# Kernel tuning notes

Measured on AMD Instinct MI355X. Metric: run time of the kernel, lower is better.

## Reference

```python
import jax, jax.numpy as jnp
import numpy as np

V = 4          # view_num
B = 2048       # batch_size
D = 512        # feature dim
N = V * B
TEMP = 0.5     # temperature
EPS = 1e-8     # torch CosineSimilarity eps


def _neg_idx():
    # Row with residue p (position within its view block) masks out columns c
    # with c % B == p (the positive/self positions), exactly matching
    # mask_positive_samples: fill_diagonal_(0) on every BxB block.
    cols = np.arange(N)
    return np.stack([cols[cols % B != p] for p in range(B)])  # [B, N-V]

_NEG_IDX = jnp.asarray(_neg_idx())


def setup_inputs() -> dict:
    key = jax.random.key(0)
    x = jax.random.normal(key, (V, B, D), dtype=jnp.float32)
    return {"x": x}


def reference(x):
    # torch.cat(input, dim=0) -> [N, D]
    xf = x.reshape(N, D)
    # Cosine similarity via normalize + matmul (same math as broadcasted
    # CosineSimilarity(dim=2), expressed efficiently).
    norm = jnp.maximum(jnp.linalg.norm(xf, axis=1, keepdims=True), EPS)
    xn = xf / norm
    sim = (xn @ xn.T) / TEMP                                  # [N, N]

    # Negatives per anchor row: gather masked columns (same column order as
    # torch boolean-mask indexing, which is row-major ascending).
    sim_v = sim.reshape(V, B, N)
    negs = jnp.take_along_axis(sim_v, _NEG_IDX[None], axis=2)  # [V, B, N-V]
    lse_neg = jax.nn.logsumexp(negs, axis=2)                   # [V, B]

    # pos[i, j, b] = sim block-diagonal between views i and j
    pos = jnp.diagonal(sim.reshape(V, B, V, B), axis1=1, axis2=3)  # [V, V, B]

    # CrossEntropy with label 0 on logits = [pos_ij, negatives_i]:
    #   loss_b = logsumexp([pos, negs]) - pos = logaddexp(pos, lse_neg) - pos
    lse = jnp.logaddexp(pos, lse_neg[:, None, :])              # [V, V, B]
    per_pair = (lse - pos).sum(axis=2) / B                     # [V, V]

    off_diag = 1.0 - jnp.eye(V, dtype=per_pair.dtype)          # skip j == i
    return jnp.sum(per_pair * off_diag)
```

## Files before the change

kernel.cpp:

```cpp
#include <hip/hip_runtime.h>
#include <hip/hip_fp8.h>

#define NV 4
#define NB 2048
#define ND 512
#define NN 8192

typedef int int8v __attribute__((ext_vector_type(8)));
typedef int int4v __attribute__((ext_vector_type(4)));
typedef float floatx4 __attribute__((ext_vector_type(4)));
#define SCALE1 0x7F7F7F7Fu

__global__ __launch_bounds__(256) void normalize_k(const float* __restrict__ x,
                                                   unsigned char* __restrict__ xn,
                                                   float* __restrict__ sumexp,
                                                   float* __restrict__ out) {
  if (threadIdx.x < 4) sumexp[blockIdx.x * 4 + threadIdx.x] = 0.0f;
  if (blockIdx.x == 0 && threadIdx.x == 0) out[0] = 0.0f;

  const int row = blockIdx.x * 4 + (threadIdx.x >> 6);
  const int l = threadIdx.x & 63;
  const float4* xr = (const float4*)(x + (size_t)row * ND);
  float4 v0 = xr[l * 2 + 0];
  float4 v1 = xr[l * 2 + 1];
  float ss = v0.x * v0.x + v0.y * v0.y + v0.z * v0.z + v0.w * v0.w +
             v1.x * v1.x + v1.y * v1.y + v1.z * v1.z + v1.w * v1.w;
#pragma unroll
  for (int off = 32; off > 0; off >>= 1) ss += __shfl_xor(ss, off, 64);
  const float inv = 1.0f / fmaxf(sqrtf(ss), 1e-8f);
  union { unsigned char b[8]; uint2 u; } pk;
  pk.b[0] = __hip_fp8_e4m3(v0.x * inv).__x;
  pk.b[1] = __hip_fp8_e4m3(v0.y * inv).__x;
  pk.b[2] = __hip_fp8_e4m3(v0.z * inv).__x;
  pk.b[3] = __hip_fp8_e4m3(v0.w * inv).__x;
  pk.b[4] = __hip_fp8_e4m3(v1.x * inv).__x;
  pk.b[5] = __hip_fp8_e4m3(v1.y * inv).__x;
  pk.b[6] = __hip_fp8_e4m3(v1.z * inv).__x;
  pk.b[7] = __hip_fp8_e4m3(v1.w * inv).__x;
  *(uint2*)(xn + (size_t)row * ND + l * 8) = pk.u;
}

__global__ __launch_bounds__(256) void sim_k(const unsigned char* __restrict__ xn,
                                             float* __restrict__ sumexp,
                                             float* __restrict__ pos) {
  __shared__ unsigned char As[128 * 128];
  __shared__ unsigned char Bs[128 * 128];
  const int tid = threadIdx.x;
  const int l = tid & 63;
  const int m = l & 15, q = l >> 4, s = l & 7;
  const int wr = (tid >> 6) >> 1, wc = (tid >> 6) & 1;

  const int bid = blockIdx.x;
  int rt = (int)((129.0f - sqrtf(16641.0f - 8.0f * (float)bid)) * 0.5f);
  rt = rt < 0 ? 0 : (rt > 63 ? 63 : rt);
  while (rt > 0 && (rt * 64 - rt * (rt - 1) / 2) > bid) --rt;
  while (rt < 63 && ((rt + 1) * 64 - (rt + 1) * rt / 2) <= bid) ++rt;
  const int ct = rt + (bid - (rt * 64 - rt * (rt - 1) / 2));
  const bool diag = (rt == ct);

  floatx4 acc[4][4] = {};

  const unsigned char* gA = xn + (size_t)rt * 128 * ND;
  const unsigned char* gB = xn + (size_t)ct * 128 * ND;

  const int crow = tid >> 3;
  const int coff = (tid & 7) * 16;
  const int lsw = ((tid & 7) ^ ((tid >> 3) & 7)) * 16;

  const int fo0 = ((2 * q + 0) ^ s) * 16;
  const int fo1 = ((2 * q + 1) ^ s) * 16;

  int4v pA[4], pB[4];
#pragma unroll
  for (int i = 0; i < 4; ++i) {
    const size_t go = (size_t)(i * 32 + crow) * ND + coff;
    pA[i] = *(const int4v*)(gA + go);
    pB[i] = *(const int4v*)(gB + go);
  }

#pragma unroll 1
  for (int kt = 0; kt < 4; ++kt) {
#pragma unroll
    for (int i = 0; i < 4; ++i) {
      const int la = (i * 32 + crow) * 128 + lsw;
      *(int4v*)(As + la) = pA[i];
      *(int4v*)(Bs + la) = pB[i];
    }
    __syncthreads();
    if (kt < 3) {
      const int kb = (kt + 1) * 128;
#pragma unroll
      for (int i = 0; i < 4; ++i) {
        const size_t go = (size_t)(i * 32 + crow) * ND + kb + coff;
        pA[i] = *(const int4v*)(gA + go);
        pB[i] = *(const int4v*)(gB + go);
      }
    }
    int8v af0, af1, af2, af3, bf0, bf1, bf2, bf3;
    {
      const unsigned char* pa0 = As + (wr * 64 + 0 * 16 + m) * 128;
      const unsigned char* pa1 = As + (wr * 64 + 1 * 16 + m) * 128;
      const unsigned char* pa2 = As + (wr * 64 + 2 * 16 + m) * 128;
      const unsigned char* pa3 = As + (wr * 64 + 3 * 16 + m) * 128;
      const unsigned char* pb0 = Bs + (wc * 64 + 0 * 16 + m) * 128;
      const unsigned char* pb1 = Bs + (wc * 64 + 1 * 16 + m) * 128;
      const unsigned char* pb2 = Bs + (wc * 64 + 2 * 16 + m) * 128;
      const unsigned char* pb3 = Bs + (wc * 64 + 3 * 16 + m) * 128;
      af0 = __builtin_shufflevector(*(const int4v*)(pa0 + fo0),
                                    *(const int4v*)(pa0 + fo1), 0,1,2,3,4,5,6,7);
      af1 = __builtin_shufflevector(*(const int4v*)(pa1 + fo0),
                                    *(const int4v*)(pa1 + fo1), 0,1,2,3,4,5,6,7);
      af2 = __builtin_shufflevector(*(const int4v*)(pa2 + fo0),
                                    *(const int4v*)(pa2 + fo1), 0,1,2,3,4,5,6,7);
      af3 = __builtin_shufflevector(*(const int4v*)(pa3 + fo0),
                                    *(const int4v*)(pa3 + fo1), 0,1,2,3,4,5,6,7);
      bf0 = __builtin_shufflevector(*(const int4v*)(pb0 + fo0),
                                    *(const int4v*)(pb0 + fo1), 0,1,2,3,4,5,6,7);
      bf1 = __builtin_shufflevector(*(const int4v*)(pb1 + fo0),
                                    *(const int4v*)(pb1 + fo1), 0,1,2,3,4,5,6,7);
      bf2 = __builtin_shufflevector(*(const int4v*)(pb2 + fo0),
                                    *(const int4v*)(pb2 + fo1), 0,1,2,3,4,5,6,7);
      bf3 = __builtin_shufflevector(*(const int4v*)(pb3 + fo0),
                                    *(const int4v*)(pb3 + fo1), 0,1,2,3,4,5,6,7);
    }
#define MFMA_ROW(mt, afv)                                                     \
  acc[mt][0] = __builtin_amdgcn_mfma_scale_f32_16x16x128_f8f6f4(              \
      afv, bf0, acc[mt][0], 0, 0, 0, SCALE1, 0, SCALE1);                      \
  acc[mt][1] = __builtin_amdgcn_mfma_scale_f32_16x16x128_f8f6f4(              \
      afv, bf1, acc[mt][1], 0, 0, 0, SCALE1, 0, SCALE1);                      \
  acc[mt][2] = __builtin_amdgcn_mfma_scale_f32_16x16x128_f8f6f4(              \
      afv, bf2, acc[mt][2], 0, 0, 0, SCALE1, 0, SCALE1);                      \
  acc[mt][3] = __builtin_amdgcn_mfma_scale_f32_16x16x128_f8f6f4(              \
      afv, bf3, acc[mt][3], 0, 0, 0, SCALE1, 0, SCALE1)
    MFMA_ROW(0, af0);
    MFMA_ROW(1, af1);
    MFMA_ROW(2, af2);
    MFMA_ROW(3, af3);
#undef MFMA_ROW
    __syncthreads();
  }

  const int r0 = rt * 128 + wr * 64;
  const int c0 = ct * 128 + wc * 64;
  float cs[4] = {0.f, 0.f, 0.f, 0.f};
#pragma unroll
  for (int mt = 0; mt < 4; ++mt) {
    float rs[4] = {0.f, 0.f, 0.f, 0.f};
#pragma unroll
    for (int nt = 0; nt < 4; ++nt) {
      const int c = c0 + nt * 16 + m;
#pragma unroll
      for (int reg = 0; reg < 4; ++reg) {
        const int r = r0 + mt * 16 + q * 4 + reg;
        const float sv = acc[mt][nt][reg] * 2.0f;
        if (((c - r) & (NB - 1)) == 0) {
          pos[r * NV + (c >> 11)] = sv;
          if (!diag) pos[c * NV + (r >> 11)] = sv;
        } else {
          const float e = __expf(sv);
          rs[reg] += e;
          cs[nt] += e;
        }
      }
    }
#pragma unroll
    for (int off = 1; off < 16; off <<= 1) {
#pragma unroll
      for (int reg = 0; reg < 4; ++reg) rs[reg] += __shfl_xor(rs[reg], off, 64);
    }
    if (m < 4) atomicAdd(&sumexp[r0 + mt * 16 + q * 4 + m], rs[m]);
  }
  if (!diag) {
#pragma unroll
    for (int nt = 0; nt < 4; ++nt) {
      cs[nt] += __shfl_xor(cs[nt], 16, 64);
      cs[nt] += __shfl_xor(cs[nt], 32, 64);
    }
    if (q == 0) {
#pragma unroll
      for (int nt = 0; nt < 4; ++nt)
        atomicAdd(&sumexp[c0 + nt * 16 + m], cs[nt]);
    }
  }
}

__global__ __launch_bounds__(256) void finalize_k(
    const float* __restrict__ sumexp, const float* __restrict__ pos,
    float* __restrict__ out) {
  const int r = blockIdx.x * 256 + threadIdx.x;
  const float se = sumexp[r];
  const int i = r >> 11;
  float local = 0.0f;
#pragma unroll
  for (int j = 0; j < NV; ++j) {
    if (j == i) continue;
    const float p = pos[r * NV + j];
    local += logf(__expf(p) + se) - p;
  }
  local *= (1.0f / NB);
#pragma unroll
  for (int off = 32; off > 0; off >>= 1) local += __shfl_xor(local, off, 64);
  if ((threadIdx.x & 63) == 0) atomicAdd(out, local);
}

extern "C" void kernel_launch(void* const* d_in, const int* in_sizes, int n_in,
                              void* d_out, int out_size, void* d_ws,
                              size_t ws_size, hipStream_t stream) {
  const float* x = (const float*)d_in[0];
  float* out = (float*)d_out;
  char* ws = (char*)d_ws;
  unsigned char* xn = (unsigned char*)ws;
  float* sumexp = (float*)(ws + (size_t)NN * ND);
  float* pos = (float*)(ws + (size_t)NN * ND + NN * 4);

  normalize_k<<<NN / 4, 256, 0, stream>>>(x, xn, sumexp, out);
  sim_k<<<64 * 65 / 2, 256, 0, stream>>>(xn, sumexp, pos);
  finalize_k<<<NN / 256, 256, 0, stream>>>(sumexp, pos, out);
}
```

Before: 110.4 us.

## Use single-wave 64x64 triangular tiles with no barriers and shared diagonal loads

The similarity kernel moves from 256-thread blocks computing 128x128 tiles to 64-thread single-wavefront blocks computing 64x64 tiles over a 128x128 upper-triangular grid. With one wave per block the __syncthreads calls are removed, and diagonal tiles load only the A panel and reuse it as B. This gives many more, smaller blocks and cuts barrier stalls, at the cost of less operand reuse per loaded byte and more atomic adds into the row sums.

Result: slower. 114.7 us (+3.9%).

```diff
diff --git a/kernel.cpp b/kernel.cpp
--- a/kernel.cpp
+++ b/kernel.cpp
@@ -40,72 +40,70 @@
   *(uint2*)(xn + (size_t)row * ND + l * 8) = pk.u;
 }
 
-__global__ __launch_bounds__(256) void sim_k(const unsigned char* __restrict__ xn,
-                                             float* __restrict__ sumexp,
-                                             float* __restrict__ pos) {
-  __shared__ unsigned char As[128 * 128];
-  __shared__ unsigned char Bs[128 * 128];
-  const int tid = threadIdx.x;
-  const int l = tid & 63;
+__global__ __launch_bounds__(64, 2) void sim_k(const unsigned char* __restrict__ xn,
+                                               float* __restrict__ sumexp,
+                                               float* __restrict__ pos) {
+  __shared__ unsigned char As[64 * 128];
+  __shared__ unsigned char Bs[64 * 128];
+  const int l = threadIdx.x;
   const int m = l & 15, q = l >> 4, s = l & 7;
-  const int wr = (tid >> 6) >> 1, wc = (tid >> 6) & 1;
 
   const int bid = blockIdx.x;
-  int rt = (int)((129.0f - sqrtf(16641.0f - 8.0f * (float)bid)) * 0.5f);
-  rt = rt < 0 ? 0 : (rt > 63 ? 63 : rt);
-  while (rt > 0 && (rt * 64 - rt * (rt - 1) / 2) > bid) --rt;
-  while (rt < 63 && ((rt + 1) * 64 - (rt + 1) * rt / 2) <= bid) ++rt;
-  const int ct = rt + (bid - (rt * 64 - rt * (rt - 1) / 2));
+  int rt = (int)((257.0f - sqrtf(66049.0f - 8.0f * (float)bid)) * 0.5f);
+  rt = rt < 0 ? 0 : (rt > 127 ? 127 : rt);
+  while (rt > 0 && (rt * 128 - rt * (rt - 1) / 2) > bid) --rt;
+  while (rt < 127 && ((rt + 1) * 128 - (rt + 1) * rt / 2) <= bid) ++rt;
+  const int ct = rt + (bid - (rt * 128 - rt * (rt - 1) / 2));
   const bool diag = (rt == ct);
 
   floatx4 acc[4][4] = {};
 
-  const unsigned char* gA = xn + (size_t)rt * 128 * ND;
-  const unsigned char* gB = xn + (size_t)ct * 128 * ND;
-
-  const int crow = tid >> 3;
-  const int coff = (tid & 7) * 16;
-  const int lsw = ((tid & 7) ^ ((tid >> 3) & 7)) * 16;
+  const unsigned char* gA = xn + (size_t)rt * 64 * ND;
+  const unsigned char* gB = xn + (size_t)ct * 64 * ND;
+
+  const int crow = l >> 3;
+  const int coff = (l & 7) * 16;
+  const int la = crow * 128 + ((l & 7) ^ crow) * 16;
 
   const int fo0 = ((2 * q + 0) ^ s) * 16;
   const int fo1 = ((2 * q + 1) ^ s) * 16;
 
-  int4v pA[4], pB[4];
-#pragma unroll
-  for (int i = 0; i < 4; ++i) {
-    const size_t go = (size_t)(i * 32 + crow) * ND + coff;
+  int4v pA[8], pB[8];
+#pragma unroll
+  for (int i = 0; i < 8; ++i) {
+    const size_t go = (size_t)(i * 8 + crow) * ND + coff;
     pA[i] = *(const int4v*)(gA + go);
-    pB[i] = *(const int4v*)(gB + go);
+    if (!diag) pB[i] = *(const int4v*)(gB + go);
   }
 
 #pragma unroll 1
   for (int kt = 0; kt < 4; ++kt) {
 #pragma unroll
-    for (int i = 0; i < 4; ++i) {
-      const int la = (i * 32 + crow) * 128 + lsw;
-      *(int4v*)(As + la) = pA[i];
-      *(int4v*)(Bs + la) = pB[i];
-    }
-    __syncthreads();
+    for (int i = 0; i < 8; ++i) {
+      *(int4v*)(As + i * 1024 + la) = pA[i];
+      if (!diag) *(int4v*)(Bs + i * 1024 + la) = pB[i];
+    }
     if (kt < 3) {
       const int kb = (kt + 1) * 128;
 #pragma unroll
-      for (int i = 0; i < 4; ++i) {
-        const size_t go = (size_t)(i * 32 + crow) * ND + kb + coff;
+      for (int i = 0; i < 8; ++i) {
+        const size_t go = (size_t)(i * 8 + crow) * ND + kb + coff;
         pA[i] = *(const int4v*)(gA + go);
-        pB[i] = *(const int4v*)(gB + go);
+        if (!diag) pB[i] = *(const int4v*)(gB + go);
       }
     }
+    const unsigned char* Ab = As;
+    const unsigned char* Bb = diag ? As : Bs;
     int8v af0, af1, af2, af3, bf0, bf1, bf2, bf3;
     {
-      const unsigned char* pa0 = As + (wr * 64 + 0 * 16 + m) * 128;
-      const unsigned char* pa1 = As + (wr * 64 + 1 * 16 + m) * 128;
-      const unsigned char* pa2 = As + (wr * 64 + 2 * 16 + m) * 128;
-      const unsigned char* pa3 = As + (wr * 64 + 3 * 16 + m) * 128;
-      const unsigned char* pb0 = Bs + (wc * 64 + 0 * 16 + m) * 128;
-      const unsigned char* pb1 = Bs + (wc * 64 + 1 * 16 + m) * 128;
-      const unsigned char* pb2 = Bs + (wc * 64 + 2 * 16 + m) * 128;
-      const unsigned char* pb3 = Bs + (wc * 64 + 3 * 16 + m) * 128;
+      const unsigned char* pa0 = Ab + (0 * 16 + m) * 128;
+      const unsigned char* pa1 = Ab + (1 * 16 + m) * 128;
+      const unsigned char* pa2 = Ab + (2 * 16 + m) * 128;
+      const unsigned char* pa3 = Ab + (3 * 16 + m) * 128;
+      const unsigned char* pb0 = Bb + (0 * 16 + m) * 128;
+      const unsigned char* pb1 = Bb + (1 * 16 + m) * 128;
+      const unsigned char* pb2 = Bb + (2 * 16 + m) * 128;
+      const unsigned char* pb3 = Bb + (3 * 16 + m) * 128;
       af0 = __builtin_shufflevector(*(const int4v*)(pa0 + fo0),
                                     *(const int4v*)(pa0 + fo1), 0,1,2,3,4,5,6,7);
       af1 = __builtin_shufflevector(*(const int4v*)(pa1 + fo0),
@@ -137,11 +135,10 @@
     MFMA_ROW(2, af2);
     MFMA_ROW(3, af3);
 #undef MFMA_ROW
-    __syncthreads();
-  }
-
-  const int r0 = rt * 128 + wr * 64;
-  const int c0 = ct * 128 + wc * 64;
+  }
+
+  const int r0 = rt * 64;
+  const int c0 = ct * 64;
   float cs[4] = {0.f, 0.f, 0.f, 0.f};
 #pragma unroll
   for (int mt = 0; mt < 4; ++mt) {
@@ -214,6 +211,6 @@
   float* pos = (float*)(ws + (size_t)NN * ND + NN * 4);
 
   normalize_k<<<NN / 4, 256, 0, stream>>>(x, xn, sumexp, out);
-  sim_k<<<64 * 65 / 2, 256, 0, stream>>>(xn, sumexp, pos);
+  sim_k<<<128 * 129 / 2, 64, 0, stream>>>(xn, sumexp, pos);
   finalize_k<<<NN / 256, 256, 0, stream>>>(sumexp, pos, out);
 }
```
